# Kernel optimization log

Measured on AMD Instinct MI355X. Metric: run time of the kernel, lower is better.

Reference implementation:

```python
import jax, jax.numpy as jnp
from jax import lax
import numpy as np

HID = 100  # embedding_dim == hidden_dim == 100 (hardcoded in module)
VOCAB = 128000
NUM_CLASSES = 20
SEQ_LEN = 8192


def setup_inputs() -> dict:
    key = jax.random.key(0)
    ks = jax.random.split(key, 8)
    s = 1.0 / np.sqrt(HID)
    return {
        "sequence": jax.random.randint(ks[0], (SEQ_LEN,), 0, VOCAB, dtype=jnp.int64 if jax.config.jax_enable_x64 else jnp.int32),
        "embedding": jax.random.normal(ks[1], (VOCAB, HID), dtype=jnp.float32),
        "W_ih": jax.random.uniform(ks[2], (4 * HID, HID), minval=-s, maxval=s, dtype=jnp.float32),
        "W_hh": jax.random.uniform(ks[3], (4 * HID, HID), minval=-s, maxval=s, dtype=jnp.float32),
        "b_ih": jax.random.uniform(ks[4], (4 * HID,), minval=-s, maxval=s, dtype=jnp.float32),
        "b_hh": jax.random.uniform(ks[5], (4 * HID,), minval=-s, maxval=s, dtype=jnp.float32),
        "fc_w": jax.random.uniform(ks[6], (NUM_CLASSES, HID), minval=-s, maxval=s, dtype=jnp.float32),
        "fc_b": jax.random.uniform(ks[7], (NUM_CLASSES,), minval=-s, maxval=s, dtype=jnp.float32),
    }


def reference(sequence, embedding, W_ih, W_hh, b_ih, b_hh, fc_w, fc_b):
    # embeds: [N, HID] gather from embedding table
    embeds = embedding[sequence]
    # precompute input projections for all timesteps in one GEMM: [N, 4H]
    x_proj = embeds @ W_ih.T + b_ih + b_hh

    def step(carry, xp):
        h, c = carry  # [HID], [HID]
        gates = xp + W_hh @ h  # [4H]; PyTorch gate order i, f, g, o
        i, f, g, o = jnp.split(gates, 4)
        i = jax.nn.sigmoid(i)
        f = jax.nn.sigmoid(f)
        g = jnp.tanh(g)
        o = jax.nn.sigmoid(o)
        c = f * c + i * g
        h = o * jnp.tanh(c)
        return (h, c), None

    h0 = jnp.zeros((HID,), dtype=embeds.dtype)
    c0 = jnp.zeros((HID,), dtype=embeds.dtype)
    (h_last, _), _ = lax.scan(step, (h0, c0), x_proj)
    out = h_last @ fc_w.T + fc_b  # fc on final-timestep output
    return out[None, :]  # view(1, -1)
```

## Files before the change

kernel.cpp:

```cpp
#include <hip/hip_runtime.h>

#define SEQ  8192
#define HID  100
#define G4   400
#define NCLS 20

typedef float v2f __attribute__((ext_vector_type(2)));
typedef float v4f __attribute__((ext_vector_type(4)));

__device__ __forceinline__ float fast_sigmoid(float x) {
    return 1.0f / (1.0f + __expf(-x));
}
__device__ __forceinline__ float fast_tanh(float x) {
    float e = __expf(2.0f * x);
    return 1.0f - 2.0f / (e + 1.0f);
}

__device__ __forceinline__ void wg_barrier() {
    asm volatile("s_waitcnt lgkmcnt(0)" ::: "memory");
    __builtin_amdgcn_s_barrier();
    asm volatile("" ::: "memory");
}

template<int CTRL>
__device__ __forceinline__ float dpp_add(float x) {
    int p = __builtin_amdgcn_update_dpp(0, __float_as_int(x), CTRL, 0xF, 0xF, true);
    return x + __int_as_float(p);
}
__device__ __forceinline__ float quad_allreduce(float x) {
    return dpp_add<0x4E>(dpp_add<0xB1>(x));
}

__global__ __launch_bounds__(512)
void xproj_kernel(const int* __restrict__ seq, const float* __restrict__ emb,
                  const float* __restrict__ Wih, const float* __restrict__ bih,
                  const float* __restrict__ bhh, float* __restrict__ xp)
{
    __shared__ float er[16][HID];
    const int tid = threadIdx.x;
    const int t0  = blockIdx.x * 16;

    if (tid < 400) {
        int r = tid / 25, q = tid - r * 25;
        int s = seq[t0 + r];
        *(float4*)&er[r][4 * q] = *(const float4*)&emb[(size_t)s * HID + 4 * q];
    }
    __syncthreads();

    const int row = (tid < G4) ? tid : (G4 - 1);
    const float4* wr = (const float4*)(Wih + (size_t)row * HID);
    const float bias = bih[row] + bhh[row];

    float acc[16];
    #pragma unroll
    for (int u = 0; u < 16; ++u) acc[u] = bias;

    #pragma unroll
    for (int k = 0; k < 25; ++k) {
        float4 wv = wr[k];
        #pragma unroll
        for (int u = 0; u < 16; ++u) {
            float4 ev = *(const float4*)&er[u][4 * k];
            acc[u] = fmaf(wv.x, ev.x, acc[u]);
            acc[u] = fmaf(wv.y, ev.y, acc[u]);
            acc[u] = fmaf(wv.z, ev.z, acc[u]);
            acc[u] = fmaf(wv.w, ev.w, acc[u]);
        }
    }
    if (tid < G4) {
        const int cj = row / HID, rj = row - cj * HID;
        const int pj = rj * 4 + cj;
        #pragma unroll
        for (int u = 0; u < 16; ++u)
            xp[(size_t)(t0 + u) * G4 + pj] = acc[u];
    }
}

template<int MODE>
__global__ __launch_bounds__(512)
__attribute__((amdgpu_waves_per_eu(2, 2)))
void lstm_scan(const float* xp,
               const float* __restrict__ Whh,
               const float* __restrict__ fcw,
               const float* __restrict__ fcb,
               const int* __restrict__ seq, const float* __restrict__ emb,
               const float* __restrict__ Wih, const float* __restrict__ bih,
               const float* __restrict__ bhh,
               float* __restrict__ out)
{
    __shared__ v4f h4[2][32];
    __shared__ v4f er4[25];

    const int tid = threadIdx.x;
    const int s   = tid & 3;
    const int rg  = tid >> 2;
    const int r   = (rg < HID) ? rg : (HID - 1);
    const bool live = (rg < HID);

    v4f w[4][7];
    #pragma unroll
    for (int c = 0; c < 4; ++c) {
        const float* wr = Whh + (size_t)(c * HID + r) * HID;
        #pragma unroll
        for (int j = 0; j < 7; ++j) {
            const int q = (j < 6) ? (s + 4 * j) : 24;
            v4f t = *(const v4f*)(wr + 4 * q);
            if (j == 6 && s != 0) t = (v4f){0.f, 0.f, 0.f, 0.f};
            w[c][j] = t;
        }
    }
    #pragma unroll
    for (int c = 0; c < 4; ++c)
        #pragma unroll
        for (int j = 0; j < 7; ++j)
            asm volatile("" : "+v"(w[c][j]));

    v4f bias4 = {0.f, 0.f, 0.f, 0.f};
    if constexpr (MODE == 1) {
        #pragma unroll
        for (int c = 0; c < 4; ++c)
            ((float*)&bias4)[c] = bih[c * HID + r] + bhh[c * HID + r];
    }

    if (tid < 128) ((float*)h4)[tid] = 0.0f;
    float cst = 0.0f;

    v4f xn[8];
    if constexpr (MODE == 0) {
        #pragma unroll
        for (int u = 0; u < 8; ++u)
            xn[u] = *(const v4f*)(xp + (size_t)u * G4 + 4 * r);
    }
    wg_barrier();

    #pragma unroll 1
    for (int t8 = 0; t8 < SEQ; t8 += 8) {
        #pragma unroll
        for (int u = 0; u < 8; ++u) {
            const int t = t8 + u;

            v4f xpv;
            if constexpr (MODE == 0) {
                xpv = xn[u];
                if (t + 8 < SEQ)
                    xn[u] = *(const v4f*)(xp + (size_t)(t + 8) * G4 + 4 * r);
            } else {
                xpv = bias4;
                if (tid < 25) {
                    int sq = seq[t];
                    er4[tid] = *(const v4f*)(emb + (size_t)sq * HID + 4 * tid);
                }
                wg_barrier();
            }

            const v4f* hb = h4[t & 1];
            v2f a0 = {0.f,0.f}, a1 = {0.f,0.f}, a2 = {0.f,0.f}, a3 = {0.f,0.f};
            #pragma unroll
            for (int j = 0; j < 7; ++j) {
                const int q = (j < 6) ? (s + 4 * j) : 24;
                v4f hv = hb[q];
                a0 = __builtin_elementwise_fma(w[0][j].lo, hv.lo, a0);
                a0 = __builtin_elementwise_fma(w[0][j].hi, hv.hi, a0);
                a1 = __builtin_elementwise_fma(w[1][j].lo, hv.lo, a1);
                a1 = __builtin_elementwise_fma(w[1][j].hi, hv.hi, a1);
                a2 = __builtin_elementwise_fma(w[2][j].lo, hv.lo, a2);
                a2 = __builtin_elementwise_fma(w[2][j].hi, hv.hi, a2);
                a3 = __builtin_elementwise_fma(w[3][j].lo, hv.lo, a3);
                a3 = __builtin_elementwise_fma(w[3][j].hi, hv.hi, a3);
            }

            if constexpr (MODE == 1) {
                #pragma unroll
                for (int c = 0; c < 4; ++c) {
                    const float* xr = Wih + (size_t)(c * HID + r) * HID;
                    #pragma unroll
                    for (int j = 0; j < 7; ++j) {
                        if (j == 6 && s != 0) continue;
                        const int q = (j < 6) ? (s + 4 * j) : 24;
                        v4f wq = *(const v4f*)(xr + 4 * q);
                        v4f ev = er4[q];
                        v2f* ac = (c == 0) ? &a0 : (c == 1) ? &a1 : (c == 2) ? &a2 : &a3;
                        *ac = __builtin_elementwise_fma(wq.lo, ev.lo, *ac);
                        *ac = __builtin_elementwise_fma(wq.hi, ev.hi, *ac);
                    }
                }
            }

            float gi = quad_allreduce(a0.x + a0.y) + xpv.x;
            float gf = quad_allreduce(a1.x + a1.y) + xpv.y;
            float gg = quad_allreduce(a2.x + a2.y) + xpv.z;
            float go = quad_allreduce(a3.x + a3.y) + xpv.w;

            gi = fast_sigmoid(gi);
            gf = fast_sigmoid(gf);
            gg = fast_tanh(gg);
            go = fast_sigmoid(go);

            cst = fmaf(gf, cst, gi * gg);
            float hn = go * fast_tanh(cst);
            if (live && s == 0)
                ((float*)h4[(t & 1) ^ 1])[r] = hn;
            wg_barrier();
        }
    }

    if (tid < NCLS) {
        const float* hf = (const float*)h4[0];
        const float* fr = fcw + (size_t)tid * HID;
        float acc = fcb[tid];
        #pragma unroll
        for (int k = 0; k < HID; ++k) acc = fmaf(fr[k], hf[k], acc);
        out[tid] = acc;
    }
}

extern "C" void kernel_launch(void* const* d_in, const int* in_sizes, int n_in,
                              void* d_out, int out_size, void* d_ws, size_t ws_size,
                              hipStream_t stream)
{
    const int*   seq = (const int*)d_in[0];
    const float* emb = (const float*)d_in[1];
    const float* Wih = (const float*)d_in[2];
    const float* Whh = (const float*)d_in[3];
    const float* bih = (const float*)d_in[4];
    const float* bhh = (const float*)d_in[5];
    const float* fcw = (const float*)d_in[6];
    const float* fcb = (const float*)d_in[7];
    float* out = (float*)d_out;
    float* xp  = (float*)d_ws;

    const size_t need = (size_t)SEQ * G4 * sizeof(float);
    if (ws_size >= need) {
        xproj_kernel<<<SEQ / 16, 512, 0, stream>>>(seq, emb, Wih, bih, bhh, xp);
        lstm_scan<0><<<1, 512, 0, stream>>>(xp, Whh, fcw, fcb,
                                            seq, emb, Wih, bih, bhh, out);
    } else {
        lstm_scan<1><<<1, 512, 0, stream>>>(nullptr, Whh, fcw, fcb,
                                            seq, emb, Wih, bih, bhh, out);
    }
}
```

Measured before the change: 5.868 ms.

## Shrink scan block to 256 threads and stage xproj chunks in LDS

The recurrent kernel now uses 256 threads with two lanes per hidden unit instead of four, so each gate reduction needs one DPP step and each thread holds 13 float4 weight slices per gate. Precomputed input projections are prefetched in chunks of 32 timesteps into double-buffered shared memory through registers, replacing per-step global loads. The goal is to cut per-step barrier and reduction cost, since 4 waves synchronize instead of 8. The trade-off is much higher register pressure at one wave per EU and longer serial FMA chains per thread.

Result: slower. 6.899 ms (+17.6%).

```diff
diff --git a/kernel.cpp b/kernel.cpp
--- a/kernel.cpp
+++ b/kernel.cpp
@@ -1,9 +1,11 @@
 #include <hip/hip_runtime.h>
 
-#define SEQ  8192
-#define HID  100
-#define G4   400
-#define NCLS 20
+#define SEQ   8192
+#define HID   100
+#define G4    400
+#define NCLS  20
+#define CH    32
+#define NCH   (SEQ / CH)
 
 typedef float v2f __attribute__((ext_vector_type(2)));
 typedef float v4f __attribute__((ext_vector_type(4)));
@@ -22,13 +24,9 @@
     asm volatile("" ::: "memory");
 }
 
-template<int CTRL>
-__device__ __forceinline__ float dpp_add(float x) {
-    int p = __builtin_amdgcn_update_dpp(0, __float_as_int(x), CTRL, 0xF, 0xF, true);
+__device__ __forceinline__ float pair_add(float x) {
+    int p = __builtin_amdgcn_update_dpp(0, __float_as_int(x), 0xB1, 0xF, 0xF, true);
     return x + __int_as_float(p);
-}
-__device__ __forceinline__ float quad_allreduce(float x) {
-    return dpp_add<0x4E>(dpp_add<0xB1>(x));
 }
 
 __global__ __launch_bounds__(512)
@@ -77,42 +75,46 @@
 }
 
 template<int MODE>
-__global__ __launch_bounds__(512)
-__attribute__((amdgpu_waves_per_eu(2, 2)))
+__global__ __launch_bounds__(256)
+__attribute__((amdgpu_waves_per_eu(1, 1)))
 void lstm_scan(const float* xp,
                const float* __restrict__ Whh,
-               const float* __restrict__ fcw,
-               const float* __restrict__ fcb,
+               const float* __restrict__ fcw, const float* __restrict__ fcb,
                const int* __restrict__ seq, const float* __restrict__ emb,
                const float* __restrict__ Wih, const float* __restrict__ bih,
                const float* __restrict__ bhh,
                float* __restrict__ out)
 {
     __shared__ v4f h4[2][32];
+    __shared__ v4f xb[2][CH * HID];
     __shared__ v4f er4[25];
 
     const int tid = threadIdx.x;
-    const int s   = tid & 3;
-    const int rg  = tid >> 2;
+    const int s   = tid & 1;
+    const int rg  = tid >> 1;
     const int r   = (rg < HID) ? rg : (HID - 1);
     const bool live = (rg < HID);
 
-    v4f w[4][7];
+    int qi[13];
+    #pragma unroll
+    for (int j = 0; j < 13; ++j)
+        qi[j] = s ? (12 + j) : ((j < 12) ? j : 24);
+
+    v4f w[4][13];
     #pragma unroll
     for (int c = 0; c < 4; ++c) {
         const float* wr = Whh + (size_t)(c * HID + r) * HID;
         #pragma unroll
-        for (int j = 0; j < 7; ++j) {
-            const int q = (j < 6) ? (s + 4 * j) : 24;
-            v4f t = *(const v4f*)(wr + 4 * q);
-            if (j == 6 && s != 0) t = (v4f){0.f, 0.f, 0.f, 0.f};
+        for (int j = 0; j < 13; ++j) {
+            v4f t = *(const v4f*)(wr + 4 * qi[j]);
+            if (s == 0 && j == 12) t = (v4f){0.f, 0.f, 0.f, 0.f};
             w[c][j] = t;
         }
     }
     #pragma unroll
     for (int c = 0; c < 4; ++c)
         #pragma unroll
-        for (int j = 0; j < 7; ++j)
+        for (int j = 0; j < 13; ++j)
             asm volatile("" : "+v"(w[c][j]));
 
     v4f bias4 = {0.f, 0.f, 0.f, 0.f};
@@ -125,71 +127,112 @@
     if (tid < 128) ((float*)h4)[tid] = 0.0f;
     float cst = 0.0f;
 
-    v4f xn[8];
     if constexpr (MODE == 0) {
-        #pragma unroll
-        for (int u = 0; u < 8; ++u)
-            xn[u] = *(const v4f*)(xp + (size_t)u * G4 + 4 * r);
-    }
-    wg_barrier();
-
-    #pragma unroll 1
-    for (int t8 = 0; t8 < SEQ; t8 += 8) {
-        #pragma unroll
-        for (int u = 0; u < 8; ++u) {
-            const int t = t8 + u;
-
-            v4f xpv;
-            if constexpr (MODE == 0) {
-                xpv = xn[u];
-                if (t + 8 < SEQ)
-                    xn[u] = *(const v4f*)(xp + (size_t)(t + 8) * G4 + 4 * r);
-            } else {
-                xpv = bias4;
-                if (tid < 25) {
-                    int sq = seq[t];
-                    er4[tid] = *(const v4f*)(emb + (size_t)sq * HID + 4 * tid);
+        const v4f* src = (const v4f*)xp;
+        #pragma unroll
+        for (int k = 0; k < 13; ++k) {
+            int slot = tid + 256 * k;
+            if (slot < CH * HID) xb[0][slot] = src[slot];
+        }
+    }
+    __syncthreads();
+
+    if constexpr (MODE == 0) {
+        #pragma unroll 1
+        for (int c = 0; c < NCH; ++c) {
+            const int cur = c & 1;
+            const bool more = (c + 1 < NCH);
+
+            v4f g[13];
+            if (more) {
+                const v4f* src = (const v4f*)xp + (size_t)(c + 1) * (CH * HID);
+                #pragma unroll
+                for (int k = 0; k < 12; ++k) g[k] = src[tid + 256 * k];
+                if (tid < CH * HID - 256 * 12)
+                    g[12] = src[tid + 256 * 12];
+            }
+
+            const v4f* xrow = &xb[cur][r];
+            #pragma unroll 1
+            for (int u8 = 0; u8 < CH; u8 += 8) {
+                #pragma unroll
+                for (int v = 0; v < 8; ++v) {
+                    const v4f* hb = h4[v & 1];
+                    v4f xpv = xrow[(u8 + v) * HID];
+
+                    v2f a0 = {0.f,0.f}, a1 = {0.f,0.f};
+                    v2f a2 = {0.f,0.f}, a3 = {0.f,0.f};
+                    #pragma unroll
+                    for (int j = 0; j < 13; ++j) {
+                        v4f hv = hb[qi[j]];
+                        a0 = __builtin_elementwise_fma(w[0][j].lo, hv.lo, a0);
+                        a0 = __builtin_elementwise_fma(w[0][j].hi, hv.hi, a0);
+                        a1 = __builtin_elementwise_fma(w[1][j].lo, hv.lo, a1);
+                        a1 = __builtin_elementwise_fma(w[1][j].hi, hv.hi, a1);
+                        a2 = __builtin_elementwise_fma(w[2][j].lo, hv.lo, a2);
+                        a2 = __builtin_elementwise_fma(w[2][j].hi, hv.hi, a2);
+                        a3 = __builtin_elementwise_fma(w[3][j].lo, hv.lo, a3);
+                        a3 = __builtin_elementwise_fma(w[3][j].hi, hv.hi, a3);
+                    }
+
+                    float gi = pair_add(a0.x + a0.y) + xpv.x;
+                    float gf = pair_add(a1.x + a1.y) + xpv.y;
+                    float gg = pair_add(a2.x + a2.y) + xpv.z;
+                    float go = pair_add(a3.x + a3.y) + xpv.w;
+
+                    gi = fast_sigmoid(gi);
+                    gf = fast_sigmoid(gf);
+                    gg = fast_tanh(gg);
+                    go = fast_sigmoid(go);
+
+                    cst = fmaf(gf, cst, gi * gg);
+                    float hn = go * fast_tanh(cst);
+                    if (live && s == 0)
+                        ((float*)h4[(v & 1) ^ 1])[r] = hn;
+                    wg_barrier();
                 }
+            }
+
+            if (more) {
+                #pragma unroll
+                for (int k = 0; k < 12; ++k)
+                    xb[cur ^ 1][tid + 256 * k] = g[k];
+                if (tid < CH * HID - 256 * 12)
+                    xb[cur ^ 1][tid + 256 * 12] = g[12];
                 wg_barrier();
             }
+        }
+    } else {
+        #pragma unroll 1
+        for (int t = 0; t < SEQ; ++t) {
+            if (tid < 25) {
+                int sq = seq[t];
+                er4[tid] = *(const v4f*)(emb + (size_t)sq * HID + 4 * tid);
+            }
+            wg_barrier();
 
             const v4f* hb = h4[t & 1];
             v2f a0 = {0.f,0.f}, a1 = {0.f,0.f}, a2 = {0.f,0.f}, a3 = {0.f,0.f};
             #pragma unroll
-            for (int j = 0; j < 7; ++j) {
-                const int q = (j < 6) ? (s + 4 * j) : 24;
-                v4f hv = hb[q];
-                a0 = __builtin_elementwise_fma(w[0][j].lo, hv.lo, a0);
-                a0 = __builtin_elementwise_fma(w[0][j].hi, hv.hi, a0);
-                a1 = __builtin_elementwise_fma(w[1][j].lo, hv.lo, a1);
-                a1 = __builtin_elementwise_fma(w[1][j].hi, hv.hi, a1);
-                a2 = __builtin_elementwise_fma(w[2][j].lo, hv.lo, a2);
-                a2 = __builtin_elementwise_fma(w[2][j].hi, hv.hi, a2);
-                a3 = __builtin_elementwise_fma(w[3][j].lo, hv.lo, a3);
-                a3 = __builtin_elementwise_fma(w[3][j].hi, hv.hi, a3);
-            }
-
-            if constexpr (MODE == 1) {
+            for (int j = 0; j < 13; ++j) {
+                v4f hv = hb[qi[j]];
+                v4f ev = er4[qi[j]];
                 #pragma unroll
                 for (int c = 0; c < 4; ++c) {
-                    const float* xr = Wih + (size_t)(c * HID + r) * HID;
-                    #pragma unroll
-                    for (int j = 0; j < 7; ++j) {
-                        if (j == 6 && s != 0) continue;
-                        const int q = (j < 6) ? (s + 4 * j) : 24;
-                        v4f wq = *(const v4f*)(xr + 4 * q);
-                        v4f ev = er4[q];
-                        v2f* ac = (c == 0) ? &a0 : (c == 1) ? &a1 : (c == 2) ? &a2 : &a3;
-                        *ac = __builtin_elementwise_fma(wq.lo, ev.lo, *ac);
-                        *ac = __builtin_elementwise_fma(wq.hi, ev.hi, *ac);
-                    }
+                    v4f wq = *(const v4f*)(Wih + (size_t)(c * HID + r) * HID + 4 * qi[j]);
+                    if (s == 0 && j == 12) wq = (v4f){0.f, 0.f, 0.f, 0.f};
+                    v2f* ac = (c == 0) ? &a0 : (c == 1) ? &a1 : (c == 2) ? &a2 : &a3;
+                    *ac = __builtin_elementwise_fma(w[c][j].lo, hv.lo, *ac);
+                    *ac = __builtin_elementwise_fma(w[c][j].hi, hv.hi, *ac);
+                    *ac = __builtin_elementwise_fma(wq.lo, ev.lo, *ac);
+                    *ac = __builtin_elementwise_fma(wq.hi, ev.hi, *ac);
                 }
             }
 
-            float gi = quad_allreduce(a0.x + a0.y) + xpv.x;
-            float gf = quad_allreduce(a1.x + a1.y) + xpv.y;
-            float gg = quad_allreduce(a2.x + a2.y) + xpv.z;
-            float go = quad_allreduce(a3.x + a3.y) + xpv.w;
+            float gi = pair_add(a0.x + a0.y) + ((float*)&bias4)[0];
+            float gf = pair_add(a1.x + a1.y) + ((float*)&bias4)[1];
+            float gg = pair_add(a2.x + a2.y) + ((float*)&bias4)[2];
+            float go = pair_add(a3.x + a3.y) + ((float*)&bias4)[3];
 
             gi = fast_sigmoid(gi);
             gf = fast_sigmoid(gf);
@@ -232,10 +275,10 @@
     const size_t need = (size_t)SEQ * G4 * sizeof(float);
     if (ws_size >= need) {
         xproj_kernel<<<SEQ / 16, 512, 0, stream>>>(seq, emb, Wih, bih, bhh, xp);
-        lstm_scan<0><<<1, 512, 0, stream>>>(xp, Whh, fcw, fcb,
+        lstm_scan<0><<<1, 256, 0, stream>>>(xp, Whh, fcw, fcb,
                                             seq, emb, Wih, bih, bhh, out);
     } else {
-        lstm_scan<1><<<1, 512, 0, stream>>>(nullptr, Whh, fcw, fcb,
+        lstm_scan<1><<<1, 256, 0, stream>>>(nullptr, Whh, fcw, fcb,
                                             seq, emb, Wih, bih, bhh, out);
     }
 }
```

## Pack two hidden units per quad in LSTM scan to use 256 threads

Applied to the files above, without the earlier changes.

The main scan kernel now assigns two hidden units to each group of four lanes, so the workgroup shrinks from 512 to 256 threads (four waves instead of eight). Each thread keeps twice as many recurrent weights in registers, 56 v4f. The x-projection output layout is interleaved so each quad reads its eight gate values with two contiguous v4f loads. Fewer waves should make each per-step barrier cheaper, at the cost of more serial FMA work per thread and high register pressure. The fallback path is split into a separate simplified kernel.

Result: slower. 7.698 ms (+31.2%).

```diff
diff --git a/kernel.cpp b/kernel.cpp
--- a/kernel.cpp
+++ b/kernel.cpp
@@ -69,24 +69,133 @@
     }
     if (tid < G4) {
         const int cj = row / HID, rj = row - cj * HID;
-        const int pj = rj * 4 + cj;
+        const int pj = (rj >> 1) * 8 + (rj & 1) * 4 + cj;
         #pragma unroll
         for (int u = 0; u < 16; ++u)
             xp[(size_t)(t0 + u) * G4 + pj] = acc[u];
     }
 }
 
-template<int MODE>
+__global__ __launch_bounds__(256, 1)
+void lstm_scan(const float* xp,
+               const float* __restrict__ Whh,
+               const float* __restrict__ fcw, const float* __restrict__ fcb,
+               float* __restrict__ out)
+{
+    __shared__ v4f h4[2][32];
+
+    const int tid = threadIdx.x;
+    const int s   = tid & 3;
+    const int g   = tid >> 2;
+    const int gc  = (g < 50) ? g : 49;
+    const bool live = (g < 50);
+
+    int qi[7];
+    #pragma unroll
+    for (int j = 0; j < 7; ++j) qi[j] = (j < 6) ? (s + 4 * j) : 24;
+
+    v4f w[8][7];
+    #pragma unroll
+    for (int p = 0; p < 2; ++p)
+        #pragma unroll
+        for (int c = 0; c < 4; ++c) {
+            const float* wr = Whh + (size_t)(c * HID + 2 * gc + p) * HID;
+            #pragma unroll
+            for (int j = 0; j < 7; ++j) {
+                v4f t = *(const v4f*)(wr + 4 * qi[j]);
+                if (s != 0 && j == 6) t = (v4f){0.f, 0.f, 0.f, 0.f};
+                w[p * 4 + c][j] = t;
+            }
+        }
+    #pragma unroll
+    for (int k = 0; k < 8; ++k)
+        #pragma unroll
+        for (int j = 0; j < 7; ++j)
+            asm volatile("" : "+v"(w[k][j]));
+
+    if (tid < 128) ((float*)h4)[tid] = 0.0f;
+    float c0 = 0.0f, c1 = 0.0f;
+
+    v4f xn[8][2];
+    #pragma unroll
+    for (int u = 0; u < 8; ++u) {
+        xn[u][0] = *(const v4f*)(xp + (size_t)u * G4 + 8 * gc);
+        xn[u][1] = *(const v4f*)(xp + (size_t)u * G4 + 8 * gc + 4);
+    }
+    wg_barrier();
+
+    #pragma unroll 1
+    for (int t8 = 0; t8 < SEQ; t8 += 8) {
+        #pragma unroll
+        for (int u = 0; u < 8; ++u) {
+            const int t = t8 + u;
+            v4f xa = xn[u][0], xb = xn[u][1];
+            if (t + 8 < SEQ) {
+                xn[u][0] = *(const v4f*)(xp + (size_t)(t + 8) * G4 + 8 * gc);
+                xn[u][1] = *(const v4f*)(xp + (size_t)(t + 8) * G4 + 8 * gc + 4);
+            }
+
+            const v4f* hb = h4[u & 1];
+            v2f aL[8], aH[8];
+            #pragma unroll
+            for (int k = 0; k < 8; ++k) { aL[k] = (v2f){0.f, 0.f}; aH[k] = (v2f){0.f, 0.f}; }
+            #pragma unroll
+            for (int j = 0; j < 7; ++j) {
+                v4f hv = hb[qi[j]];
+                #pragma unroll
+                for (int k = 0; k < 8; ++k) {
+                    aL[k] = __builtin_elementwise_fma(w[k][j].lo, hv.lo, aL[k]);
+                    aH[k] = __builtin_elementwise_fma(w[k][j].hi, hv.hi, aH[k]);
+                }
+            }
+
+            float G[8];
+            #pragma unroll
+            for (int k = 0; k < 8; ++k) {
+                v2f t2 = aL[k] + aH[k];
+                G[k] = quad_allreduce(t2.x + t2.y);
+            }
+            G[0] += xa.x; G[1] += xa.y; G[2] += xa.z; G[3] += xa.w;
+            G[4] += xb.x; G[5] += xb.y; G[6] += xb.z; G[7] += xb.w;
+
+            float i0 = fast_sigmoid(G[0]);
+            float f0 = fast_sigmoid(G[1]);
+            float g0 = fast_tanh(G[2]);
+            float o0 = fast_sigmoid(G[3]);
+            c0 = fmaf(f0, c0, i0 * g0);
+            float h0 = o0 * fast_tanh(c0);
+            float i1 = fast_sigmoid(G[4]);
+            float f1 = fast_sigmoid(G[5]);
+            float g1 = fast_tanh(G[6]);
+            float o1 = fast_sigmoid(G[7]);
+            c1 = fmaf(f1, c1, i1 * g1);
+            float h1 = o1 * fast_tanh(c1);
+
+            if (live && s == 0) {
+                float2 hw = make_float2(h0, h1);
+                *(float2*)&((float*)h4[(u & 1) ^ 1])[2 * gc] = hw;
+            }
+            wg_barrier();
+        }
+    }
+
+    if (tid < NCLS) {
+        const float* hf = (const float*)h4[0];
+        const float* fr = fcw + (size_t)tid * HID;
+        float acc = fcb[tid];
+        #pragma unroll
+        for (int k = 0; k < HID; ++k) acc = fmaf(fr[k], hf[k], acc);
+        out[tid] = acc;
+    }
+}
+
 __global__ __launch_bounds__(512)
 __attribute__((amdgpu_waves_per_eu(2, 2)))
-void lstm_scan(const float* xp,
-               const float* __restrict__ Whh,
-               const float* __restrict__ fcw,
-               const float* __restrict__ fcb,
-               const int* __restrict__ seq, const float* __restrict__ emb,
-               const float* __restrict__ Wih, const float* __restrict__ bih,
-               const float* __restrict__ bhh,
-               float* __restrict__ out)
+void lstm_scan_small(const int* __restrict__ seq, const float* __restrict__ emb,
+                     const float* __restrict__ Wih, const float* __restrict__ Whh,
+                     const float* __restrict__ bih, const float* __restrict__ bhh,
+                     const float* __restrict__ fcw, const float* __restrict__ fcb,
+                     float* __restrict__ out)
 {
     __shared__ v4f h4[2][32];
     __shared__ v4f er4[25];
@@ -97,111 +206,71 @@
     const int r   = (rg < HID) ? rg : (HID - 1);
     const bool live = (rg < HID);
 
+    int qi[7];
+    #pragma unroll
+    for (int j = 0; j < 7; ++j) qi[j] = (j < 6) ? (s + 4 * j) : 24;
+
     v4f w[4][7];
     #pragma unroll
     for (int c = 0; c < 4; ++c) {
         const float* wr = Whh + (size_t)(c * HID + r) * HID;
         #pragma unroll
         for (int j = 0; j < 7; ++j) {
-            const int q = (j < 6) ? (s + 4 * j) : 24;
-            v4f t = *(const v4f*)(wr + 4 * q);
-            if (j == 6 && s != 0) t = (v4f){0.f, 0.f, 0.f, 0.f};
+            v4f t = *(const v4f*)(wr + 4 * qi[j]);
+            if (s != 0 && j == 6) t = (v4f){0.f, 0.f, 0.f, 0.f};
             w[c][j] = t;
         }
     }
+
+    v4f bias4;
     #pragma unroll
     for (int c = 0; c < 4; ++c)
-        #pragma unroll
-        for (int j = 0; j < 7; ++j)
-            asm volatile("" : "+v"(w[c][j]));
-
-    v4f bias4 = {0.f, 0.f, 0.f, 0.f};
-    if constexpr (MODE == 1) {
-        #pragma unroll
-        for (int c = 0; c < 4; ++c)
-            ((float*)&bias4)[c] = bih[c * HID + r] + bhh[c * HID + r];
-    }
+        ((float*)&bias4)[c] = bih[c * HID + r] + bhh[c * HID + r];
 
     if (tid < 128) ((float*)h4)[tid] = 0.0f;
     float cst = 0.0f;
-
-    v4f xn[8];
-    if constexpr (MODE == 0) {
-        #pragma unroll
-        for (int u = 0; u < 8; ++u)
-            xn[u] = *(const v4f*)(xp + (size_t)u * G4 + 4 * r);
-    }
-    wg_barrier();
+    __syncthreads();
 
     #pragma unroll 1
-    for (int t8 = 0; t8 < SEQ; t8 += 8) {
-        #pragma unroll
-        for (int u = 0; u < 8; ++u) {
-            const int t = t8 + u;
-
-            v4f xpv;
-            if constexpr (MODE == 0) {
-                xpv = xn[u];
-                if (t + 8 < SEQ)
-                    xn[u] = *(const v4f*)(xp + (size_t)(t + 8) * G4 + 4 * r);
-            } else {
-                xpv = bias4;
-                if (tid < 25) {
-                    int sq = seq[t];
-                    er4[tid] = *(const v4f*)(emb + (size_t)sq * HID + 4 * tid);
-                }
-                wg_barrier();
-            }
-
-            const v4f* hb = h4[t & 1];
-            v2f a0 = {0.f,0.f}, a1 = {0.f,0.f}, a2 = {0.f,0.f}, a3 = {0.f,0.f};
-            #pragma unroll
-            for (int j = 0; j < 7; ++j) {
-                const int q = (j < 6) ? (s + 4 * j) : 24;
-                v4f hv = hb[q];
-                a0 = __builtin_elementwise_fma(w[0][j].lo, hv.lo, a0);
-                a0 = __builtin_elementwise_fma(w[0][j].hi, hv.hi, a0);
-                a1 = __builtin_elementwise_fma(w[1][j].lo, hv.lo, a1);
-                a1 = __builtin_elementwise_fma(w[1][j].hi, hv.hi, a1);
-                a2 = __builtin_elementwise_fma(w[2][j].lo, hv.lo, a2);
-                a2 = __builtin_elementwise_fma(w[2][j].hi, hv.hi, a2);
-                a3 = __builtin_elementwise_fma(w[3][j].lo, hv.lo, a3);
-                a3 = __builtin_elementwise_fma(w[3][j].hi, hv.hi, a3);
-            }
-
-            if constexpr (MODE == 1) {
-                #pragma unroll
-                for (int c = 0; c < 4; ++c) {
-                    const float* xr = Wih + (size_t)(c * HID + r) * HID;
-                    #pragma unroll
-                    for (int j = 0; j < 7; ++j) {
-                        if (j == 6 && s != 0) continue;
-                        const int q = (j < 6) ? (s + 4 * j) : 24;
-                        v4f wq = *(const v4f*)(xr + 4 * q);
-                        v4f ev = er4[q];
-                        v2f* ac = (c == 0) ? &a0 : (c == 1) ? &a1 : (c == 2) ? &a2 : &a3;
-                        *ac = __builtin_elementwise_fma(wq.lo, ev.lo, *ac);
-                        *ac = __builtin_elementwise_fma(wq.hi, ev.hi, *ac);
-                    }
-                }
-            }
-
-            float gi = quad_allreduce(a0.x + a0.y) + xpv.x;
-            float gf = quad_allreduce(a1.x + a1.y) + xpv.y;
-            float gg = quad_allreduce(a2.x + a2.y) + xpv.z;
-            float go = quad_allreduce(a3.x + a3.y) + xpv.w;
-
-            gi = fast_sigmoid(gi);
-            gf = fast_sigmoid(gf);
-            gg = fast_tanh(gg);
-            go = fast_sigmoid(go);
-
-            cst = fmaf(gf, cst, gi * gg);
-            float hn = go * fast_tanh(cst);
-            if (live && s == 0)
-                ((float*)h4[(t & 1) ^ 1])[r] = hn;
-            wg_barrier();
-        }
+    for (int t = 0; t < SEQ; ++t) {
+        if (tid < 25) {
+            int sq = seq[t];
+            er4[tid] = *(const v4f*)(emb + (size_t)sq * HID + 4 * tid);
+        }
+        wg_barrier();
+
+        const v4f* hb = h4[t & 1];
+        v2f a0 = {0.f,0.f}, a1 = {0.f,0.f}, a2 = {0.f,0.f}, a3 = {0.f,0.f};
+        #pragma unroll
+        for (int j = 0; j < 7; ++j) {
+            v4f hv = hb[qi[j]];
+            v4f ev = er4[qi[j]];
+            #pragma unroll
+            for (int c = 0; c < 4; ++c) {
+                v4f wq = *(const v4f*)(Wih + (size_t)(c * HID + r) * HID + 4 * qi[j]);
+                if (s != 0 && j == 6) wq = (v4f){0.f, 0.f, 0.f, 0.f};
+                v2f* ac = (c == 0) ? &a0 : (c == 1) ? &a1 : (c == 2) ? &a2 : &a3;
+                *ac = __builtin_elementwise_fma(w[c][j].lo, hv.lo, *ac);
+                *ac = __builtin_elementwise_fma(w[c][j].hi, hv.hi, *ac);
+                *ac = __builtin_elementwise_fma(wq.lo, ev.lo, *ac);
+                *ac = __builtin_elementwise_fma(wq.hi, ev.hi, *ac);
+            }
+        }
+        float gi = quad_allreduce(a0.x + a0.y) + ((float*)&bias4)[0];
+        float gf = quad_allreduce(a1.x + a1.y) + ((float*)&bias4)[1];
+        float gg = quad_allreduce(a2.x + a2.y) + ((float*)&bias4)[2];
+        float go = quad_allreduce(a3.x + a3.y) + ((float*)&bias4)[3];
+
+        gi = fast_sigmoid(gi);
+        gf = fast_sigmoid(gf);
+        gg = fast_tanh(gg);
+        go = fast_sigmoid(go);
+
+        cst = fmaf(gf, cst, gi * gg);
+        float hn = go * fast_tanh(cst);
+        if (live && s == 0)
+            ((float*)h4[(t & 1) ^ 1])[r] = hn;
+        wg_barrier();
     }
 
     if (tid < NCLS) {
@@ -232,10 +301,9 @@
     const size_t need = (size_t)SEQ * G4 * sizeof(float);
     if (ws_size >= need) {
         xproj_kernel<<<SEQ / 16, 512, 0, stream>>>(seq, emb, Wih, bih, bhh, xp);
-        lstm_scan<0><<<1, 512, 0, stream>>>(xp, Whh, fcw, fcb,
-                                            seq, emb, Wih, bih, bhh, out);
+        lstm_scan<<<1, 256, 0, stream>>>(xp, Whh, fcw, fcb, out);
     } else {
-        lstm_scan<1><<<1, 512, 0, stream>>>(nullptr, Whh, fcw, fcb,
-                                            seq, emb, Wih, bih, bhh, out);
-    }
-}
+        lstm_scan_small<<<1, 512, 0, stream>>>(seq, emb, Wih, Whh,
+                                               bih, bhh, fcw, fcb, out);
+    }
+}
```
